# Kernel optimization log

Hardware: AMD Instinct MI355X
Metric: run time of the kernel (lower is better)

The kernel has to match this reference:

```python
import jax, jax.numpy as jnp
import numpy as np

B, T, F_DIM, H = 4096, 64, 128, 128
LAM = 0.5  # lambda_spurious

def _gelu(x):
    return jax.nn.gelu(x, approximate=False)  # torch nn.GELU default = exact erf

def _ln(x, g, b):
    m = x.mean(-1, keepdims=True)
    v = ((x - m) ** 2).mean(-1, keepdims=True)
    return (x - m) / jnp.sqrt(v + 1e-5) * g + b

def _lin_init(k, fan_in, fan_out):
    kw, kb = jax.random.split(k)
    s = 1.0 / np.sqrt(fan_in)
    w = jax.random.uniform(kw, (fan_in, fan_out), minval=-s, maxval=s, dtype=jnp.float32)
    b = jax.random.uniform(kb, (fan_out,), minval=-s, maxval=s, dtype=jnp.float32)
    return w, b

def setup_inputs() -> dict:
    key = jax.random.key(0)
    ks = jax.random.split(key, 16)
    inp = {}
    inp['causal_summary'] = jax.random.normal(ks[0], (B, T, F_DIM), dtype=jnp.float32)
    inp['spurious_summary'] = jax.random.normal(ks[1], (B, T, F_DIM), dtype=jnp.float32)
    inp['labels'] = jax.random.randint(ks[2], (B,), 0, 2)
    inp['valid_mask'] = jax.random.bernoulli(ks[3], 0.7, (B, T))
    inp['ce_w1'], inp['ce_b1'] = _lin_init(ks[4], F_DIM, H)
    inp['ce_w2'], inp['ce_b2'] = _lin_init(ks[5], H, H)
    inp['se_w1'], inp['se_b1'] = _lin_init(ks[6], F_DIM, H)
    inp['se_w2'], inp['se_b2'] = _lin_init(ks[7], H, H)
    inp['cd_g'] = jnp.ones((H,), jnp.float32); inp['cd_b'] = jnp.zeros((H,), jnp.float32)
    inp['cd_w1'], inp['cd_b1'] = _lin_init(ks[8], H, H)
    inp['cd_w2'], inp['cd_b2'] = _lin_init(ks[9], H, 2)
    inp['jd_g'] = jnp.ones((2 * H,), jnp.float32); inp['jd_b'] = jnp.zeros((2 * H,), jnp.float32)
    inp['jd_w1'], inp['jd_b1'] = _lin_init(ks[10], 2 * H, H)
    inp['jd_w2'], inp['jd_b2'] = _lin_init(ks[11], H, 2)
    return inp

def _forward(causal_summary, spurious_summary, labels, valid_mask, params):
    (ce_w1, ce_b1, ce_w2, ce_b2, se_w1, se_b1, se_w2, se_b2,
     cd_g, cd_b, cd_w1, cd_b1, cd_w2, cd_b2,
     jd_g, jd_b, jd_w1, jd_b1, jd_w2, jd_b2) = params
    enc = lambda x, w1, b1, w2, b2: _gelu(x @ w1 + b1) @ w2 + b2
    c_rep = enc(causal_summary, ce_w1, ce_b1, ce_w2, ce_b2)    # [B,T,H]
    s_rep = enc(spurious_summary, se_w1, se_b1, se_w2, se_b2)  # [B,T,H]
    dec = lambda x, g, b, w1, b1, w2, b2: _gelu(_ln(x, g, b) @ w1 + b1) @ w2 + b2
    logits_c = dec(c_rep, cd_g, cd_b, cd_w1, cd_b1, cd_w2, cd_b2)  # [B,T,2]
    logits_j = dec(jnp.concatenate([c_rep, s_rep], -1), jd_g, jd_b, jd_w1, jd_b1, jd_w2, jd_b2)
    onehot = jax.nn.one_hot(labels, 2, dtype=jnp.float32)      # [B,2]
    # per-sample cross entropy: logsumexp - logit[label]
    ce_c = jax.nn.logsumexp(logits_c, -1) - jnp.einsum('btk,bk->bt', logits_c, onehot)
    ce_j = jax.nn.logsumexp(logits_j, -1) - jnp.einsum('btk,bk->bt', logits_j, onehot)
    mask_f = valid_mask.astype(jnp.float32)                    # [B,T]
    counts = jnp.einsum('bt,bk->tk', mask_f, onehot)           # per-step active label counts
    tot = counts.sum(-1)                                       # [T]
    probs = counts / jnp.clip(tot, 1.0, None)[:, None]
    ent = -(probs * jnp.log(probs + 1e-8)).sum(-1)             # [T] label entropy per step
    step_valid = (tot >= 2.0).astype(jnp.float32)              # torch skips steps with active.sum() < 2
    mi_c = ent[None, :] - ce_c                                 # mutual information estimate
    cond = jnp.maximum(ce_c - ce_j, 0.0)                       # == clamp(mi_joint - mi_c, 0)
    reward = mask_f * step_valid[None, :] * (mi_c - LAM * cond)
    denom = jnp.clip(tot, 1.0, None)
    aux_step = 0.5 * ((mask_f * ce_c).sum(0) + (mask_f * ce_j).sum(0)) / denom  # mean of (aux_c, aux_joint)
    n_valid = step_valid.sum()
    aux_loss = jnp.where(n_valid > 0, (step_valid * aux_step).sum() / jnp.maximum(n_valid, 1.0), 0.0)
    return reward, aux_loss

def reference(causal_summary, spurious_summary, labels, valid_mask,
              ce_w1, ce_b1, ce_w2, ce_b2, se_w1, se_b1, se_w2, se_b2,
              cd_g, cd_b, cd_w1, cd_b1, cd_w2, cd_b2,
              jd_g, jd_b, jd_w1, jd_b1, jd_w2, jd_b2):
    params = (ce_w1, ce_b1, ce_w2, ce_b2, se_w1, se_b1, se_w2, se_b2,
              cd_g, cd_b, cd_w1, cd_b1, cd_w2, cd_b2,
              jd_g, jd_b, jd_w1, jd_b1, jd_w2, jd_b2)
    return _forward(causal_summary, spurious_summary, labels, valid_mask, params)
```

## Files before the change

kernel.cpp:

```cpp
#include <hip/hip_runtime.h>
#include <hip/hip_fp16.h>

#define B_ 4096
#define T_ 64
#define NROWS (B_*T_)
#define BLOB_B 2099200
#define PIMG_B (BLOB_B + 7*32768)

typedef _Float16 f16x8 __attribute__((ext_vector_type(8)));
typedef float    f32x4 __attribute__((ext_vector_type(4)));

__device__ __forceinline__ float gelu_f(float x){
    float u = 0.7978845608028654f * (x + 0.044715f * x * x * x);
    float t = 1.f - 2.f / (__expf(2.f * u) + 1.f);
    return 0.5f * x * (1.f + t);
}

__device__ __forceinline__ void gll16(const void* g, void* l){
    __builtin_amdgcn_global_load_lds(
        (const __attribute__((address_space(1))) void*)g,
        (__attribute__((address_space(3))) void*)l, 16, 0, 0);
}

__device__ __forceinline__ void stage_w(const char* gsrc, char* wbuf, int wave, int lane){
    const char* g = gsrc + wave * 8192 + lane * 16;
    char* l = wbuf + wave * 8192;
#pragma unroll
    for (int r = 0; r < 8; r++) gll16(g + r * 1024, l + r * 1024);
}

__device__ __forceinline__ void stage_p(const char* gsrc, char* sp, int wave, int lane){
    gll16(gsrc + wave * 1024 + lane * 16, sp + wave * 1024);
}

__device__ __forceinline__ void load_in(f16x8* a, const float* __restrict__ p, int g){
#pragma unroll
    for (int ks = 0; ks < 4; ks++){
        const float* q = p + ks * 32 + g * 8;
        float4 v0 = *(const float4*)q, v1 = *(const float4*)(q + 4);
        f16x8 t;
        t[0]=(_Float16)v0.x; t[1]=(_Float16)v0.y; t[2]=(_Float16)v0.z; t[3]=(_Float16)v0.w;
        t[4]=(_Float16)v1.x; t[5]=(_Float16)v1.y; t[6]=(_Float16)v1.z; t[7]=(_Float16)v1.w;
        a[ks] = t;
    }
}

__device__ __forceinline__ void load_a(f16x8* a, const char* ab, int c, int g){
    const int rswz = (c & 7) << 4;
    const char* rp = ab + c * 256;
#pragma unroll
    for (int ks = 0; ks < 4; ks++)
        a[ks] = *(const f16x8*)(rp + ((ks * 64 + g * 16) ^ rswz));
}

__device__ __forceinline__ void mfma_tile(f32x4* acc, const f16x8* a,
                                          const unsigned short* wb, int c, int g){
#pragma unroll
    for (int n = 0; n < 8; n++){
        const int r = n * 16 + c;
        const char* rp = (const char*)wb + r * 256;
        const int swz = (r & 7) << 4;
#pragma unroll
        for (int ks = 0; ks < 4; ks++){
            f16x8 b = *(const f16x8*)(rp + ((ks * 64 + g * 16) ^ swz));
            acc[n] = __builtin_amdgcn_mfma_f32_16x16x32_f16(a[ks], b, acc[n], 0, 0, 0);
        }
    }
}

__device__ __forceinline__ void build_y(f16x8* y, const f16x8* x, float mu, float rs,
                                        const unsigned short* sbh, int goff, int boff, int g){
#pragma unroll
    for (int ks = 0; ks < 4; ks++){
        f16x8 gam = *(const f16x8*)((const char*)sbh + goff * 2 + ks * 64 + g * 16);
        f16x8 bet = *(const f16x8*)((const char*)sbh + boff * 2 + ks * 64 + g * 16);
        f16x8 t;
#pragma unroll
        for (int j = 0; j < 8; j++){
            float v = ((float)x[ks][j] - mu) * rs * (float)gam[j] + (float)bet[j];
            t[j] = (_Float16)v;
        }
        y[ks] = t;
    }
}

__device__ __forceinline__ void logits_ce(const f32x4* acc, const unsigned short* sbh,
                                          int b1off, int w2off, const float* __restrict__ b2,
                                          int c, int g, int lab, float* ce){
    const _Float16* sbf = (const _Float16*)sbh;
    float l0[4] = {0,0,0,0}, l1[4] = {0,0,0,0};
#pragma unroll
    for (int n = 0; n < 8; n++){
        const int r = n * 16 + c;
        float b1v = (float)sbf[b1off + r];
        float wx  = (float)sbf[w2off + 2 * r];
        float wy  = (float)sbf[w2off + 2 * r + 1];
#pragma unroll
        for (int rr = 0; rr < 4; rr++){
            float hv = gelu_f(acc[n][rr] + b1v);
            l0[rr] += hv * wx; l1[rr] += hv * wy;
        }
    }
    const float b2x = b2[0], b2y = b2[1];
#pragma unroll
    for (int rr = 0; rr < 4; rr++){
#pragma unroll
        for (int m = 1; m < 16; m <<= 1){ l0[rr] += __shfl_xor(l0[rr], m); l1[rr] += __shfl_xor(l1[rr], m); }
        float v0 = l0[rr] + b2x, v1 = l1[rr] + b2y;
        float mx = fmaxf(v0, v1);
        float lse = mx + logf(expf(v0 - mx) + expf(v1 - mx));
        ce[rr] = lse - (lab ? v1 : v0);
    }
}

__global__ void k_prep(const float* __restrict__ ce_w1, const float* __restrict__ ce_w2,
                       const float* __restrict__ se_w1, const float* __restrict__ se_w2,
                       const float* __restrict__ cd_w1, const float* __restrict__ jd_w1,
                       const float* __restrict__ ce_b1, const float* __restrict__ ce_b2,
                       const float* __restrict__ se_b1, const float* __restrict__ se_b2,
                       const float* __restrict__ cd_g,  const float* __restrict__ cd_bt,
                       const float* __restrict__ cd_b1, const float* __restrict__ jd_g,
                       const float* __restrict__ jd_bt, const float* __restrict__ jd_b1,
                       const float* __restrict__ cd_w2, const float* __restrict__ jd_w2,
                       float* __restrict__ ws){
    char* blob = (char*)ws + BLOB_B;
    const int bid = blockIdx.x, tid = threadIdx.x;
    if (bid < 448){
        int e = bid * 256 + tid;
        int m = e >> 14, idx = e & 16383;
        int k = idx >> 7, cc = idx & 127;
        const float* src;
        switch (m){
            case 0: src = ce_w1; break;
            case 1: src = ce_w2; break;
            case 2: src = se_w1; break;
            case 3: src = se_w2; break;
            case 4: src = cd_w1; break;
            case 5: src = jd_w1; break;
            default: src = jd_w1 + 128 * 128; break;
        }
        float v = src[k * 128 + cc];
        int byte = m * 32768 + cc * 256 + ((k << 1) ^ ((cc & 7) << 4));
        *(_Float16*)(blob + byte) = (_Float16)v;
    } else {
        _Float16* p = (_Float16*)((char*)ws + PIMG_B);
        if (tid < 128){
            p[tid]       = (_Float16)ce_b1[tid]; p[128 + tid] = (_Float16)ce_b2[tid];
            p[256 + tid] = (_Float16)se_b1[tid]; p[384 + tid] = (_Float16)se_b2[tid];
            p[512 + tid] = (_Float16)cd_g[tid];  p[640 + tid] = (_Float16)cd_bt[tid];
            p[768 + tid] = (_Float16)cd_b1[tid]; p[896 + tid] = (_Float16)jd_b1[tid];
        } else {
            int i = tid - 128;
            p[1024 + i] = (_Float16)jd_g[i];        p[1152 + i] = (_Float16)jd_g[128 + i];
            p[1280 + i] = (_Float16)jd_bt[i];       p[1408 + i] = (_Float16)jd_bt[128 + i];
            p[1536 + 2*i] = (_Float16)cd_w2[2*i];   p[1537 + 2*i] = (_Float16)cd_w2[2*i+1];
            p[1792 + 2*i] = (_Float16)jd_w2[2*i];   p[1793 + 2*i] = (_Float16)jd_w2[2*i+1];
        }
    }
}

__global__ void k_stats(const int* __restrict__ mask, const int* __restrict__ labels,
                        float* __restrict__ ws){
    int t = blockIdx.x, tid = threadIdx.x;
    float c0 = 0.f, c1 = 0.f;
    for (int b = tid; b < B_; b += 256){
        if (mask[b * T_ + t]){
            if (labels[b] == 1) c1 += 1.f; else c0 += 1.f;
        }
    }
    for (int m = 1; m < 64; m <<= 1){ c0 += __shfl_xor(c0, m); c1 += __shfl_xor(c1, m); }
    __shared__ float sh[8];
    int w = tid >> 6, l = tid & 63;
    if (l == 0){ sh[w] = c0; sh[4 + w] = c1; }
    __syncthreads();
    if (tid == 0){
        float a0 = sh[0] + sh[1] + sh[2] + sh[3];
        float a1 = sh[4] + sh[5] + sh[6] + sh[7];
        float tot = a0 + a1;
        float d = fmaxf(tot, 1.f);
        float p0 = a0 / d, p1 = a1 / d;
        float ent = -(p0 * logf(p0 + 1e-8f) + p1 * logf(p1 + 1e-8f));
        ws[t] = ent;
        ws[64 + t] = (tot >= 2.f) ? 1.f : 0.f;
        ws[128 + t] = tot;
    }
}

__global__ __launch_bounds__(256, 2) void k_main(
    const float* __restrict__ xc, const float* __restrict__ xs,
    const int* __restrict__ labels, const int* __restrict__ mask,
    const float* __restrict__ cd_b2, const float* __restrict__ jd_b2,
    float* __restrict__ ws, float* __restrict__ out)
{
    __shared__ __align__(16) unsigned short wbuf[128 * 128];
    __shared__ __align__(16) unsigned short abuf[4 * 16 * 128];
    __shared__ __align__(16) unsigned short sp[2048];

    const int tid = threadIdx.x;
    const int wave = tid >> 6, lane = tid & 63;
    const int c = lane & 15, g = lane >> 4;
    const int wrow0 = blockIdx.x * 64 + wave * 16;
    char* const ab = (char*)abuf + wave * 4096;
    const int lab = labels[(wrow0 + g * 4) >> 6];
    const char* blob = (const char*)ws + BLOB_B;

    f16x8 aX[4], a4[4], cr[4], sr[4], yb[4];
    f32x4 acc[8];
    float ceC[4], ceJ[4];
    float s0c, s1c, mcv, rcv, jmv, jrv;

    stage_p((const char*)ws + PIMG_B, (char*)sp, wave, lane);
    stage_w(blob + 0 * 32768, (char*)wbuf, wave, lane);
    load_in(aX, xc + (wrow0 + c) * 128, g);
    __syncthreads();

    const _Float16* sbf = (const _Float16*)sp;

#pragma unroll
    for (int n = 0; n < 8; n++) acc[n] = (f32x4){0.f,0.f,0.f,0.f};
    mfma_tile(acc, aX, wbuf, c, g);
#pragma unroll
    for (int n = 0; n < 8; n++){
        const int col = n * 16 + c;
        float bi = (float)sbf[col];
#pragma unroll
        for (int rr = 0; rr < 4; rr++){
            float v = gelu_f(acc[n][rr] + bi);
            int row = g * 4 + rr;
            *(_Float16*)(ab + row * 256 + ((col << 1) ^ ((row & 7) << 4))) = (_Float16)v;
        }
    }
    __syncthreads();
    stage_w(blob + 1 * 32768, (char*)wbuf, wave, lane);
    load_a(a4, ab, c, g);
    __syncthreads();

#pragma unroll
    for (int n = 0; n < 8; n++) acc[n] = (f32x4){0.f,0.f,0.f,0.f};
    mfma_tile(acc, a4, wbuf, c, g);
#pragma unroll
    for (int n = 0; n < 8; n++){
        const int col = n * 16 + c;
        float bi = (float)sbf[128 + col];
#pragma unroll
        for (int rr = 0; rr < 4; rr++){
            int row = g * 4 + rr;
            *(_Float16*)(ab + row * 256 + ((col << 1) ^ ((row & 7) << 4))) = (_Float16)(acc[n][rr] + bi);
        }
    }
    __syncthreads();
    stage_w(blob + 2 * 32768, (char*)wbuf, wave, lane);
    load_a(cr, ab, c, g);
    {
        s0c = 0.f; s1c = 0.f;
#pragma unroll
        for (int ks = 0; ks < 4; ks++)
#pragma unroll
            for (int j = 0; j < 8; j++){ float v = (float)cr[ks][j]; s0c += v; s1c += v*v; }
        s0c += __shfl_xor(s0c, 16); s0c += __shfl_xor(s0c, 32);
        s1c += __shfl_xor(s1c, 16); s1c += __shfl_xor(s1c, 32);
    }
    load_in(aX, xs + (wrow0 + c) * 128, g);
    __syncthreads();

#pragma unroll
    for (int n = 0; n < 8; n++) acc[n] = (f32x4){0.f,0.f,0.f,0.f};
    mfma_tile(acc, aX, wbuf, c, g);
#pragma unroll
    for (int n = 0; n < 8; n++){
        const int col = n * 16 + c;
        float bi = (float)sbf[256 + col];
#pragma unroll
        for (int rr = 0; rr < 4; rr++){
            float v = gelu_f(acc[n][rr] + bi);
            int row = g * 4 + rr;
            *(_Float16*)(ab + row * 256 + ((col << 1) ^ ((row & 7) << 4))) = (_Float16)v;
        }
    }
    __syncthreads();
    stage_w(blob + 3 * 32768, (char*)wbuf, wave, lane);
    load_a(a4, ab, c, g);
    __syncthreads();

#pragma unroll
    for (int n = 0; n < 8; n++) acc[n] = (f32x4){0.f,0.f,0.f,0.f};
    mfma_tile(acc, a4, wbuf, c, g);
#pragma unroll
    for (int n = 0; n < 8; n++){
        const int col = n * 16 + c;
        float bi = (float)sbf[384 + col];
#pragma unroll
        for (int rr = 0; rr < 4; rr++){
            int row = g * 4 + rr;
            *(_Float16*)(ab + row * 256 + ((col << 1) ^ ((row & 7) << 4))) = (_Float16)(acc[n][rr] + bi);
        }
    }
    __syncthreads();
    stage_w(blob + 4 * 32768, (char*)wbuf, wave, lane);
    load_a(sr, ab, c, g);
    {
        float s0s = 0.f, s1s = 0.f;
#pragma unroll
        for (int ks = 0; ks < 4; ks++)
#pragma unroll
            for (int j = 0; j < 8; j++){ float v = (float)sr[ks][j]; s0s += v; s1s += v*v; }
        s0s += __shfl_xor(s0s, 16); s0s += __shfl_xor(s0s, 32);
        s1s += __shfl_xor(s1s, 16); s1s += __shfl_xor(s1s, 32);
        mcv = s0c * (1.f/128.f);
        rcv = rsqrtf(s1c * (1.f/128.f) - mcv * mcv + 1e-5f);
        jmv = (s0c + s0s) * (1.f/256.f);
        jrv = rsqrtf((s1c + s1s) * (1.f/256.f) - jmv * jmv + 1e-5f);
    }
    __syncthreads();

    build_y(yb, cr, mcv, rcv, sp, 512, 640, g);
#pragma unroll
    for (int n = 0; n < 8; n++) acc[n] = (f32x4){0.f,0.f,0.f,0.f};
    mfma_tile(acc, yb, wbuf, c, g);
    __syncthreads();
    stage_w(blob + 5 * 32768, (char*)wbuf, wave, lane);
    logits_ce(acc, sp, 768, 1536, cd_b2, c, g, lab, ceC);
    __syncthreads();

    build_y(yb, cr, jmv, jrv, sp, 1024, 1280, g);
#pragma unroll
    for (int n = 0; n < 8; n++) acc[n] = (f32x4){0.f,0.f,0.f,0.f};
    mfma_tile(acc, yb, wbuf, c, g);
    __syncthreads();
    stage_w(blob + 6 * 32768, (char*)wbuf, wave, lane);
    build_y(yb, sr, jmv, jrv, sp, 1152, 1408, g);
    __syncthreads();

    mfma_tile(acc, yb, wbuf, c, g);
    logits_ce(acc, sp, 896, 1792, jd_b2, c, g, lab, ceJ);

    if (c == 0){
        const int rowbase = wrow0 + g * 4;
        const int4  m4 = *(const int4*)(mask + rowbase);
        const float4 e4 = *(const float4*)(ws + (rowbase & 63));
        const float4 s4 = *(const float4*)(ws + 64 + (rowbase & 63));
        const int   mm[4] = {m4.x, m4.y, m4.z, m4.w};
        const float ee[4] = {e4.x, e4.y, e4.z, e4.w};
        const float sv[4] = {s4.x, s4.y, s4.z, s4.w};
        float rw[4], mc2[4], mj2[4];
#pragma unroll
        for (int rr = 0; rr < 4; rr++){
            float mf = mm[rr] ? 1.f : 0.f;
            float cec = ceC[rr], cej = ceJ[rr];
            rw[rr]  = mf * sv[rr] * (ee[rr] - cec - 0.5f * fmaxf(cec - cej, 0.f));
            mc2[rr] = mf * cec;
            mj2[rr] = mf * cej;
        }
        *(float4*)(out + rowbase)              = (float4){rw[0], rw[1], rw[2], rw[3]};
        *(float4*)(ws + 512 + rowbase)         = (float4){mc2[0], mc2[1], mc2[2], mc2[3]};
        *(float4*)(ws + 512 + NROWS + rowbase) = (float4){mj2[0], mj2[1], mj2[2], mj2[3]};
    }
}

__global__ void k_aux1(float* __restrict__ ws){
    int t = blockIdx.x, tid = threadIdx.x;
    const float* mc = ws + 512;
    const float* mj = ws + 512 + NROWS;
    float sc = 0.f, sj = 0.f;
    for (int b = tid; b < B_; b += 256){ sc += mc[b * T_ + t]; sj += mj[b * T_ + t]; }
    for (int m = 1; m < 64; m <<= 1){ sc += __shfl_xor(sc, m); sj += __shfl_xor(sj, m); }
    __shared__ float sh[8];
    int w = tid >> 6, l = tid & 63;
    if (l == 0){ sh[w] = sc; sh[4 + w] = sj; }
    __syncthreads();
    if (tid == 0){
        float a0 = sh[0] + sh[1] + sh[2] + sh[3];
        float a1 = sh[4] + sh[5] + sh[6] + sh[7];
        ws[192 + t] = ws[64 + t] * 0.5f * (a0 + a1) / fmaxf(ws[128 + t], 1.f);
    }
}

__global__ void k_aux2(const float* __restrict__ ws, float* __restrict__ out){
    int l = threadIdx.x;
    float cv = ws[192 + l], sv = ws[64 + l];
    for (int m = 1; m < 64; m <<= 1){ cv += __shfl_xor(cv, m); sv += __shfl_xor(sv, m); }
    if (l == 0) out[NROWS] = (sv > 0.f) ? cv / fmaxf(sv, 1.f) : 0.f;
}

extern "C" void kernel_launch(void* const* d_in, const int* in_sizes, int n_in,
                              void* d_out, int out_size, void* d_ws, size_t ws_size,
                              hipStream_t stream) {
    const float* xc     = (const float*)d_in[0];
    const float* xs     = (const float*)d_in[1];
    const int*   labels = (const int*)d_in[2];
    const int*   mask   = (const int*)d_in[3];
    const float* ce_w1  = (const float*)d_in[4];
    const float* ce_b1  = (const float*)d_in[5];
    const float* ce_w2  = (const float*)d_in[6];
    const float* ce_b2  = (const float*)d_in[7];
    const float* se_w1  = (const float*)d_in[8];
    const float* se_b1  = (const float*)d_in[9];
    const float* se_w2  = (const float*)d_in[10];
    const float* se_b2  = (const float*)d_in[11];
    const float* cd_g   = (const float*)d_in[12];
    const float* cd_b   = (const float*)d_in[13];
    const float* cd_w1  = (const float*)d_in[14];
    const float* cd_b1  = (const float*)d_in[15];
    const float* cd_w2  = (const float*)d_in[16];
    const float* cd_b2  = (const float*)d_in[17];
    const float* jd_g   = (const float*)d_in[18];
    const float* jd_b   = (const float*)d_in[19];
    const float* jd_w1  = (const float*)d_in[20];
    const float* jd_b1  = (const float*)d_in[21];
    const float* jd_w2  = (const float*)d_in[22];
    const float* jd_b2  = (const float*)d_in[23];
    float* ws  = (float*)d_ws;
    float* out = (float*)d_out;

    k_prep<<<449, 256, 0, stream>>>(ce_w1, ce_w2, se_w1, se_w2, cd_w1, jd_w1,
                                    ce_b1, ce_b2, se_b1, se_b2, cd_g, cd_b,
                                    cd_b1, jd_g, jd_b, jd_b1, cd_w2, jd_w2, ws);
    k_stats<<<64, 256, 0, stream>>>(mask, labels, ws);
    k_main<<<4096, 256, 0, stream>>>(xc, xs, labels, mask, cd_b2, jd_b2, ws, out);
    k_aux1<<<64, 256, 0, stream>>>(ws);
    k_aux2<<<1, 64, 0, stream>>>(ws, out);
}
```

Before: 266.7 us.

## Overlap weight staging with epilogues, merge stats kernel into prep, drop barriers

```diff
diff --git a/kernel.cpp b/kernel.cpp
--- a/kernel.cpp
+++ b/kernel.cpp
@@ -68,6 +68,24 @@
     }
 }
 
+template<bool GELU>
+__device__ __forceinline__ void epi_store(const f32x4* acc, char* ab,
+                                          const unsigned short* sbh, int boff, int c, int g){
+    const _Float16* sbf = (const _Float16*)sbh;
+#pragma unroll
+    for (int n = 0; n < 8; n++){
+        const int col = n * 16 + c;
+        float bi = (float)sbf[boff + col];
+#pragma unroll
+        for (int rr = 0; rr < 4; rr++){
+            float v = acc[n][rr] + bi;
+            if (GELU) v = gelu_f(v);
+            int row = g * 4 + rr;
+            *(_Float16*)(ab + row * 256 + ((col << 1) ^ ((row & 7) << 4))) = (_Float16)v;
+        }
+    }
+}
+
 __device__ __forceinline__ void build_y(f16x8* y, const f16x8* x, float mu, float rs,
                                         const unsigned short* sbh, int goff, int boff, int g){
 #pragma unroll
@@ -82,6 +100,16 @@
         }
         y[ks] = t;
     }
+}
+
+__device__ __forceinline__ void row_stats(const f16x8* x, float& s0, float& s1){
+    s0 = 0.f; s1 = 0.f;
+#pragma unroll
+    for (int ks = 0; ks < 4; ks++)
+#pragma unroll
+        for (int j = 0; j < 8; j++){ float v = (float)x[ks][j]; s0 += v; s1 += v*v; }
+    s0 += __shfl_xor(s0, 16); s0 += __shfl_xor(s0, 32);
+    s1 += __shfl_xor(s1, 16); s1 += __shfl_xor(s1, 32);
 }
 
 __device__ __forceinline__ void logits_ce(const f32x4* acc, const unsigned short* sbh,
@@ -122,6 +150,7 @@
                        const float* __restrict__ cd_b1, const float* __restrict__ jd_g,
                        const float* __restrict__ jd_bt, const float* __restrict__ jd_b1,
                        const float* __restrict__ cd_w2, const float* __restrict__ jd_w2,
+                       const int* __restrict__ mask, const int* __restrict__ labels,
                        float* __restrict__ ws){
     char* blob = (char*)ws + BLOB_B;
     const int bid = blockIdx.x, tid = threadIdx.x;
@@ -142,6 +171,30 @@
         float v = src[k * 128 + cc];
         int byte = m * 32768 + cc * 256 + ((k << 1) ^ ((cc & 7) << 4));
         *(_Float16*)(blob + byte) = (_Float16)v;
+    } else if (bid < 512){
+        int t = bid - 448;
+        float c0 = 0.f, c1 = 0.f;
+        for (int b = tid; b < B_; b += 256){
+            if (mask[b * T_ + t]){
+                if (labels[b] == 1) c1 += 1.f; else c0 += 1.f;
+            }
+        }
+        for (int m = 1; m < 64; m <<= 1){ c0 += __shfl_xor(c0, m); c1 += __shfl_xor(c1, m); }
+        __shared__ float sh[8];
+        int w = tid >> 6, l = tid & 63;
+        if (l == 0){ sh[w] = c0; sh[4 + w] = c1; }
+        __syncthreads();
+        if (tid == 0){
+            float a0 = sh[0] + sh[1] + sh[2] + sh[3];
+            float a1 = sh[4] + sh[5] + sh[6] + sh[7];
+            float tot = a0 + a1;
+            float d = fmaxf(tot, 1.f);
+            float p0 = a0 / d, p1 = a1 / d;
+            float ent = -(p0 * logf(p0 + 1e-8f) + p1 * logf(p1 + 1e-8f));
+            ws[t] = ent;
+            ws[64 + t] = (tot >= 2.f) ? 1.f : 0.f;
+            ws[128 + t] = tot;
+        }
     } else {
         _Float16* p = (_Float16*)((char*)ws + PIMG_B);
         if (tid < 128){
@@ -159,33 +212,6 @@
     }
 }
 
-__global__ void k_stats(const int* __restrict__ mask, const int* __restrict__ labels,
-                        float* __restrict__ ws){
-    int t = blockIdx.x, tid = threadIdx.x;
-    float c0 = 0.f, c1 = 0.f;
-    for (int b = tid; b < B_; b += 256){
-        if (mask[b * T_ + t]){
-            if (labels[b] == 1) c1 += 1.f; else c0 += 1.f;
-        }
-    }
-    for (int m = 1; m < 64; m <<= 1){ c0 += __shfl_xor(c0, m); c1 += __shfl_xor(c1, m); }
-    __shared__ float sh[8];
-    int w = tid >> 6, l = tid & 63;
-    if (l == 0){ sh[w] = c0; sh[4 + w] = c1; }
-    __syncthreads();
-    if (tid == 0){
-        float a0 = sh[0] + sh[1] + sh[2] + sh[3];
-        float a1 = sh[4] + sh[5] + sh[6] + sh[7];
-        float tot = a0 + a1;
-        float d = fmaxf(tot, 1.f);
-        float p0 = a0 / d, p1 = a1 / d;
-        float ent = -(p0 * logf(p0 + 1e-8f) + p1 * logf(p1 + 1e-8f));
-        ws[t] = ent;
-        ws[64 + t] = (tot >= 2.f) ? 1.f : 0.f;
-        ws[128 + t] = tot;
-    }
-}
-
 __global__ __launch_bounds__(256, 2) void k_main(
     const float* __restrict__ xc, const float* __restrict__ xs,
     const int* __restrict__ labels, const int* __restrict__ mask,
@@ -214,105 +240,52 @@
     load_in(aX, xc + (wrow0 + c) * 128, g);
     __syncthreads();
 
-    const _Float16* sbf = (const _Float16*)sp;
-
 #pragma unroll
     for (int n = 0; n < 8; n++) acc[n] = (f32x4){0.f,0.f,0.f,0.f};
     mfma_tile(acc, aX, wbuf, c, g);
-#pragma unroll
-    for (int n = 0; n < 8; n++){
-        const int col = n * 16 + c;
-        float bi = (float)sbf[col];
-#pragma unroll
-        for (int rr = 0; rr < 4; rr++){
-            float v = gelu_f(acc[n][rr] + bi);
-            int row = g * 4 + rr;
-            *(_Float16*)(ab + row * 256 + ((col << 1) ^ ((row & 7) << 4))) = (_Float16)v;
-        }
-    }
     __syncthreads();
     stage_w(blob + 1 * 32768, (char*)wbuf, wave, lane);
+    epi_store<true>(acc, ab, sp, 0, c, g);
+    __syncthreads();
+
     load_a(a4, ab, c, g);
-    __syncthreads();
-
 #pragma unroll
     for (int n = 0; n < 8; n++) acc[n] = (f32x4){0.f,0.f,0.f,0.f};
     mfma_tile(acc, a4, wbuf, c, g);
-#pragma unroll
-    for (int n = 0; n < 8; n++){
-        const int col = n * 16 + c;
-        float bi = (float)sbf[128 + col];
-#pragma unroll
-        for (int rr = 0; rr < 4; rr++){
-            int row = g * 4 + rr;
-            *(_Float16*)(ab + row * 256 + ((col << 1) ^ ((row & 7) << 4))) = (_Float16)(acc[n][rr] + bi);
-        }
-    }
     __syncthreads();
     stage_w(blob + 2 * 32768, (char*)wbuf, wave, lane);
+    epi_store<false>(acc, ab, sp, 128, c, g);
+    load_in(aX, xs + (wrow0 + c) * 128, g);
+    __syncthreads();
+
     load_a(cr, ab, c, g);
-    {
-        s0c = 0.f; s1c = 0.f;
-#pragma unroll
-        for (int ks = 0; ks < 4; ks++)
-#pragma unroll
-            for (int j = 0; j < 8; j++){ float v = (float)cr[ks][j]; s0c += v; s1c += v*v; }
-        s0c += __shfl_xor(s0c, 16); s0c += __shfl_xor(s0c, 32);
-        s1c += __shfl_xor(s1c, 16); s1c += __shfl_xor(s1c, 32);
-    }
-    load_in(aX, xs + (wrow0 + c) * 128, g);
-    __syncthreads();
-
 #pragma unroll
     for (int n = 0; n < 8; n++) acc[n] = (f32x4){0.f,0.f,0.f,0.f};
     mfma_tile(acc, aX, wbuf, c, g);
-#pragma unroll
-    for (int n = 0; n < 8; n++){
-        const int col = n * 16 + c;
-        float bi = (float)sbf[256 + col];
-#pragma unroll
-        for (int rr = 0; rr < 4; rr++){
-            float v = gelu_f(acc[n][rr] + bi);
-            int row = g * 4 + rr;
-            *(_Float16*)(ab + row * 256 + ((col << 1) ^ ((row & 7) << 4))) = (_Float16)v;
-        }
-    }
     __syncthreads();
     stage_w(blob + 3 * 32768, (char*)wbuf, wave, lane);
+    epi_store<true>(acc, ab, sp, 256, c, g);
+    row_stats(cr, s0c, s1c);
+    __syncthreads();
+
     load_a(a4, ab, c, g);
-    __syncthreads();
-
 #pragma unroll
     for (int n = 0; n < 8; n++) acc[n] = (f32x4){0.f,0.f,0.f,0.f};
     mfma_tile(acc, a4, wbuf, c, g);
-#pragma unroll
-    for (int n = 0; n < 8; n++){
-        const int col = n * 16 + c;
-        float bi = (float)sbf[384 + col];
-#pragma unroll
-        for (int rr = 0; rr < 4; rr++){
-            int row = g * 4 + rr;
-            *(_Float16*)(ab + row * 256 + ((col << 1) ^ ((row & 7) << 4))) = (_Float16)(acc[n][rr] + bi);
-        }
-    }
     __syncthreads();
     stage_w(blob + 4 * 32768, (char*)wbuf, wave, lane);
+    epi_store<false>(acc, ab, sp, 384, c, g);
+    __syncthreads();
+
     load_a(sr, ab, c, g);
     {
-        float s0s = 0.f, s1s = 0.f;
-#pragma unroll
-        for (int ks = 0; ks < 4; ks++)
-#pragma unroll
-            for (int j = 0; j < 8; j++){ float v = (float)sr[ks][j]; s0s += v; s1s += v*v; }
-        s0s += __shfl_xor(s0s, 16); s0s += __shfl_xor(s0s, 32);
-        s1s += __shfl_xor(s1s, 16); s1s += __shfl_xor(s1s, 32);
+        float s0s, s1s;
+        row_stats(sr, s0s, s1s);
         mcv = s0c * (1.f/128.f);
         rcv = rsqrtf(s1c * (1.f/128.f) - mcv * mcv + 1e-5f);
         jmv = (s0c + s0s) * (1.f/256.f);
         jrv = rsqrtf((s1c + s1s) * (1.f/256.f) - jmv * jmv + 1e-5f);
     }
-    __syncthreads();
-
     build_y(yb, cr, mcv, rcv, sp, 512, 640, g);
 #pragma unroll
     for (int n = 0; n < 8; n++) acc[n] = (f32x4){0.f,0.f,0.f,0.f};
@@ -320,9 +293,9 @@
     __syncthreads();
     stage_w(blob + 5 * 32768, (char*)wbuf, wave, lane);
     logits_ce(acc, sp, 768, 1536, cd_b2, c, g, lab, ceC);
-    __syncthreads();
-
     build_y(yb, cr, jmv, jrv, sp, 1024, 1280, g);
+    __syncthreads();
+
 #pragma unroll
     for (int n = 0; n < 8; n++) acc[n] = (f32x4){0.f,0.f,0.f,0.f};
     mfma_tile(acc, yb, wbuf, c, g);
@@ -412,10 +385,10 @@
     float* ws  = (float*)d_ws;
     float* out = (float*)d_out;
 
-    k_prep<<<449, 256, 0, stream>>>(ce_w1, ce_w2, se_w1, se_w2, cd_w1, jd_w1,
+    k_prep<<<513, 256, 0, stream>>>(ce_w1, ce_w2, se_w1, se_w2, cd_w1, jd_w1,
                                     ce_b1, ce_b2, se_b1, se_b2, cd_g, cd_b,
-                                    cd_b1, jd_g, jd_b, jd_b1, cd_w2, jd_w2, ws);
-    k_stats<<<64, 256, 0, stream>>>(mask, labels, ws);
+                                    cd_b1, jd_g, jd_b, jd_b1, cd_w2, jd_w2,
+                                    mask, labels, ws);
     k_main<<<4096, 256, 0, stream>>>(xc, xs, labels, mask, cd_b2, jd_b2, ws, out);
     k_aux1<<<64, 256, 0, stream>>>(ws);
     k_aux2<<<1, 64, 0, stream>>>(ws, out);
```

New measurement: 230.6 us. 13.5% less time.
